# Performance work log

Measured on AMD Instinct MI355X. Metric: run time of the kernel, lower is better.

Reference implementation:

```python
import jax, jax.numpy as jnp
import numpy as np

K = 3      # spline order
NUM = 5    # grid intervals


def bspline_basis(x, grid, k=K):
    """Cox-de Boor recursion. x: (B, D); grid: (num+2k+1,) extended knots.
    Returns basis of shape (B, D, num+k)."""
    xe = x[..., None]                                       # (B, D, 1)
    B = ((xe >= grid[:-1]) & (xe < grid[1:])).astype(x.dtype)  # (B, D, num+2k)
    for p in range(1, k + 1):
        left = (xe - grid[:-(p + 1)]) / (grid[p:-1] - grid[:-(p + 1)])
        right = (grid[p + 1:] - xe) / (grid[p + 1:] - grid[1:-p])
        B = left * B[..., :-1] + right * B[..., 1:]
    return B                                                # (B, D, num+k)


def kan_layer(x, grid, coef, sb, sp, mask, bias):
    """phi(x)[b,o] = sum_i mask[o,i]*(sb[o,i]*silu(x[b,i]) + sp[o,i]*sum_c B[b,i,c]*coef[o,i,c]) + bias[o]"""
    Bsp = bspline_basis(x, grid)                            # (B, in, C)
    spline = jnp.einsum('bic,oic->bo', Bsp, coef * (sp * mask)[:, :, None])
    base = jnp.einsum('bi,oi->bo', jax.nn.silu(x), sb * mask)
    return base + spline + bias


def setup_inputs() -> dict:
    key = jax.random.key(0)
    ks = jax.random.split(key, 6)
    Bch, d0, d1, d2 = 8192, 1024, 2048, 1024
    C = NUM + K                                 # 8 spline coeffs per edge
    h = 2.0 / NUM                               # grid_range [-1,1]
    # extended knot vector: k extra knots each side, num+2k+1 = 12 points
    grid = jnp.arange(-K, NUM + K + 1, dtype=jnp.float32) * h - 1.0
    return {
        "x": jax.random.normal(ks[0], (Bch, d0), jnp.float32) * 0.5,
        "coef0": jax.random.normal(ks[1], (d1, d0, C), jnp.float32) * 0.1,
        "sb0": jax.random.normal(ks[2], (d1, d0), jnp.float32) / np.sqrt(d0).astype(np.float32),
        "sp0": jnp.ones((d1, d0), jnp.float32),
        "mask0": jnp.ones((d1, d0), jnp.float32),
        "bias0": jnp.zeros((d1,), jnp.float32),
        "coef1": jax.random.normal(ks[3], (d2, d1, C), jnp.float32) * 0.1,
        "sb1": jax.random.normal(ks[4], (d2, d1), jnp.float32) / np.sqrt(d1).astype(np.float32),
        "sp1": jnp.ones((d2, d1), jnp.float32),
        "mask1": jnp.ones((d2, d1), jnp.float32),
        "bias1": jnp.zeros((d2,), jnp.float32),
        "grid": grid,
    }


def reference(x, coef0, sb0, sp0, mask0, bias0, coef1, sb1, sp1, mask1, bias1, grid):
    h1 = kan_layer(x, grid, coef0, sb0, sp0, mask0, bias0)
    out = kan_layer(h1, grid, coef1, sb1, sp1, mask1, bias1)
    return out
```

## Files before the change

kernel.cpp:

```cpp
#include <hip/hip_runtime.h>
#include <hip/hip_bf16.h>
#include <cstdint>


typedef __attribute__((ext_vector_type(8))) short short8;
typedef __attribute__((ext_vector_type(4))) short short4v;
typedef __attribute__((ext_vector_type(4))) float f32x4;

#define GLD16(gp, lp)                                                          \
  __builtin_amdgcn_global_load_lds(                                           \
      (const __attribute__((address_space(1))) unsigned int*)(gp),             \
      (__attribute__((address_space(3))) unsigned int*)(lp), 16, 0, 0)

__device__ __forceinline__ unsigned short f2bf(float f) {
  __hip_bfloat16 h = __float2bfloat16(f);
  return *reinterpret_cast<unsigned short*>(&h);
}

__global__ void prep_w(const float* __restrict__ coef, const float* __restrict__ sb,
                       const float* __restrict__ sp, const float* __restrict__ mask,
                       __hip_bfloat16* __restrict__ W, int O, int I) {
  long idx = (long)blockIdx.x * blockDim.x + threadIdx.x;
  long total = (long)O * I;
  if (idx >= total) return;
  int i = (int)(idx % I);
  int o = (int)(idx / I);
  float mk  = mask[idx];
  float spm = sp[idx] * mk;
  float sbm = sb[idx] * mk;
  const float4* cf = (const float4*)(coef + (size_t)idx * 8);
  float4 c0 = cf[0], c1 = cf[1];
  __hip_bfloat16* base = W + (size_t)o * (size_t)(9 * I) + (i >> 5) * 288 + (i & 31);
  base[0 * 32] = __float2bfloat16(c0.x * spm);
  base[1 * 32] = __float2bfloat16(c0.y * spm);
  base[2 * 32] = __float2bfloat16(c0.z * spm);
  base[3 * 32] = __float2bfloat16(c0.w * spm);
  base[4 * 32] = __float2bfloat16(c1.x * spm);
  base[5 * 32] = __float2bfloat16(c1.y * spm);
  base[6 * 32] = __float2bfloat16(c1.z * spm);
  base[7 * 32] = __float2bfloat16(c1.w * spm);
  base[8 * 32] = __float2bfloat16(sbm);
}

__device__ __forceinline__ void basis8(float x, float* w, int& j) {
  float u  = (x + 2.2f) * 2.5f;
  float fj = floorf(u);
  j = (int)fj;
  float t  = u - fj;
  float omt = 1.0f - t;
  float t2 = t * t, t3 = t2 * t;
  w[0] = omt * omt * omt * (1.0f / 6.0f);
  w[1] = (3.0f * t3 - 6.0f * t2 + 4.0f) * (1.0f / 6.0f);
  w[2] = (-3.0f * t3 + 3.0f * t2 + 3.0f * t + 1.0f) * (1.0f / 6.0f);
  w[3] = t3 * (1.0f / 6.0f);
}

__global__ void expand_aug(const float* __restrict__ src,
                           __hip_bfloat16* __restrict__ aug,
                           long totalQuads, int I) {
  long idx = (long)blockIdx.x * blockDim.x + threadIdx.x;
  if (idx >= totalQuads) return;
  int  qtr = I >> 2;
  int  iq = (int)(idx % qtr);
  long b  = idx / qtr;
  int  i  = iq << 2;
  float4 xv = *(const float4*)(src + b * (size_t)I + i);

  float w[4][4], s[4];
  int   j[4];
#pragma unroll
  for (int e = 0; e < 4; e++) {
    float xe = (e == 0) ? xv.x : (e == 1) ? xv.y : (e == 2) ? xv.z : xv.w;
    s[e] = xe / (1.0f + __expf(-xe));
    basis8(xe, w[e], j[e]);
  }

  __hip_bfloat16* base = aug + b * (size_t)(9 * I) + (i >> 5) * 288 + (i & 31);
#pragma unroll
  for (int c = 0; c < 8; c++) {
    short4v pk;
#pragma unroll
    for (int e = 0; e < 4; e++) {
      int d = j[e] - c;
      float v = 0.0f;
      v = (d == 0) ? w[e][3] : v;
      v = (d == 1) ? w[e][2] : v;
      v = (d == 2) ? w[e][1] : v;
      v = (d == 3) ? w[e][0] : v;
      pk[e] = (short)f2bf(v);
    }
    *(short4v*)(base + c * 32) = pk;
  }
  short4v ps;
#pragma unroll
  for (int e = 0; e < 4; e++) ps[e] = (short)f2bf(s[e]);
  *(short4v*)(base + 8 * 32) = ps;
}

template <int BN>
__global__ __launch_bounds__(512, 2) void gemm8p(
    const __hip_bfloat16* __restrict__ A, const __hip_bfloat16* __restrict__ Bw,
    const float* __restrict__ bias, float* __restrict__ Cout, int N, int K) {
  constexpr int WN   = BN / 4;
  constexpr int NREP = BN / 64;
  constexpr int BNB  = BN * 64;
  constexpr int BUFB = 16384 + BNB;
  __shared__ __attribute__((aligned(16))) char lds[3 * BUFB];

  const int t = threadIdx.x;
  const int w = t >> 6, l = t & 63;
  const int wr = w >> 2, wc = w & 3;
  const int lr = l & 15;
  const int kbs = ((l >> 4) * 16) ^ (((lr >> 1) & 3) << 4);

  unsigned nwg = gridDim.x * gridDim.y;
  unsigned lin = blockIdx.y * gridDim.x + blockIdx.x;
  unsigned swz = (lin & 7) * (nwg >> 3) + (lin >> 3);
  unsigned bx = swz % gridDim.x, by = swz / gridDim.x;
  size_t brow = (size_t)by * 256, bcol = (size_t)bx * BN;

  f32x4 acc[8][NREP];
#pragma unroll
  for (int m = 0; m < 8; m++)
#pragma unroll
    for (int n = 0; n < NREP; n++) acc[m][n] = (f32x4){0.f, 0.f, 0.f, 0.f};

  const int srow  = t >> 2;
  const int scolb = ((t & 3) * 16) ^ (((srow >> 1) & 3) << 4);
  const __hip_bfloat16* gA0 = A + (brow + srow) * (size_t)K + (scolb >> 1);
  const __hip_bfloat16* gA1 = gA0 + (size_t)128 * K;
  const __hip_bfloat16* gB0 = Bw + (bcol + srow) * (size_t)K + (scolb >> 1);
  const __hip_bfloat16* gB1 = gB0 + (size_t)128 * K;

  char* ldsp = (char*)lds;
  const int paOff = (wr * 128 + lr) * 64 + kbs;
  const int pbOff = 16384 + (wc * WN + lr) * 64 + kbs;

  auto STAGE = [&](int kt, int q) {
    const int k = kt << 5;
    char* bp = ldsp + q * BUFB;
    GLD16(gA0 + k, bp + w * 1024);
    GLD16(gA1 + k, bp + 8192 + w * 1024);
    GLD16(gB0 + k, bp + 16384 + w * 1024);
    if constexpr (BN == 256) GLD16(gB1 + k, bp + 16384 + 8192 + w * 1024);
  };

  short8 bq[NREP], aq[4];
  auto COMPUTE = [&](int q) {
    const char* pa = ldsp + q * BUFB + paOff;
    const char* pb = ldsp + q * BUFB + pbOff;
#pragma unroll
    for (int n = 0; n < NREP; n++) bq[n] = *(const short8*)(pb + n * 1024);
#pragma unroll
    for (int m = 0; m < 4; m++) aq[m] = *(const short8*)(pa + m * 1024);
    __builtin_amdgcn_s_setprio(1);
#pragma unroll
    for (int m = 0; m < 4; m++)
#pragma unroll
      for (int n = 0; n < NREP; n++)
        acc[m][n] = __builtin_amdgcn_mfma_f32_16x16x32_bf16(aq[m], bq[n], acc[m][n], 0, 0, 0);
    __builtin_amdgcn_s_setprio(0);
#pragma unroll
    for (int m = 0; m < 4; m++) aq[m] = *(const short8*)(pa + (m + 4) * 1024);
    __builtin_amdgcn_s_setprio(1);
#pragma unroll
    for (int m = 0; m < 4; m++)
#pragma unroll
      for (int n = 0; n < NREP; n++)
        acc[m + 4][n] = __builtin_amdgcn_mfma_f32_16x16x32_bf16(aq[m], bq[n], acc[m + 4][n], 0, 0, 0);
    __builtin_amdgcn_s_setprio(0);
    __builtin_amdgcn_s_barrier();
  };

  const int NT = K >> 5;

  STAGE(0, 0);
  STAGE(1, 1);

  int q0 = 0;
  for (int kt = 0; kt < NT - 2; ++kt) {
    int q2 = q0 + 2; if (q2 >= 3) q2 -= 3;
    STAGE(kt + 2, q2);
    if constexpr (BN == 256) asm volatile("s_waitcnt vmcnt(8)" ::: "memory");
    else                     asm volatile("s_waitcnt vmcnt(6)" ::: "memory");
    __builtin_amdgcn_s_barrier();
    COMPUTE(q0);
    q0 = (q0 == 2) ? 0 : q0 + 1;
  }
  if constexpr (BN == 256) asm volatile("s_waitcnt vmcnt(4)" ::: "memory");
  else                     asm volatile("s_waitcnt vmcnt(3)" ::: "memory");
  __builtin_amdgcn_s_barrier();
  COMPUTE(q0);
  q0 = (q0 == 2) ? 0 : q0 + 1;
  asm volatile("s_waitcnt vmcnt(0)" ::: "memory");
  __builtin_amdgcn_s_barrier();
  COMPUTE(q0);

  const int orow = (l >> 4) << 2;
#pragma unroll
  for (int n = 0; n < NREP; n++) {
    size_t col = bcol + (size_t)wc * WN + n * 16 + lr;
    float bv = bias[col];
#pragma unroll
    for (int m = 0; m < 8; m++) {
      size_t row = brow + (size_t)wr * 128 + m * 16 + orow;
#pragma unroll
      for (int r = 0; r < 4; r++)
        Cout[(row + r) * (size_t)N + col] = acc[m][n][r] + bv;
    }
  }
}

extern "C" void kernel_launch(void* const* d_in, const int* in_sizes, int n_in,
                              void* d_out, int out_size, void* d_ws, size_t ws_size,
                              hipStream_t stream) {
  const float* x     = (const float*)d_in[0];
  const float* coef0 = (const float*)d_in[1];
  const float* sb0   = (const float*)d_in[2];
  const float* sp0   = (const float*)d_in[3];
  const float* mask0 = (const float*)d_in[4];
  const float* bias0 = (const float*)d_in[5];
  const float* coef1 = (const float*)d_in[6];
  const float* sb1   = (const float*)d_in[7];
  const float* sp1   = (const float*)d_in[8];
  const float* mask1 = (const float*)d_in[9];
  const float* bias1 = (const float*)d_in[10];
  float* out = (float*)d_out;

  const int B = 8192, D0 = 1024, D1 = 2048, D2 = 1024;
  const int K0 = 9 * D0;
  const int K1 = 9 * D1;

  char* ws = (char*)d_ws;
  float*          h1  = (float*)ws;
  __hip_bfloat16* W   = (__hip_bfloat16*)(ws + (size_t)67108864);
  __hip_bfloat16* Aug = (__hip_bfloat16*)(ws + (size_t)104857600);

  const bool fullL1 = ws_size >= (size_t)104857600 + (size_t)B * K1 * 2;

  {
    long nw = (long)D1 * D0;
    prep_w<<<(unsigned)((nw + 255) / 256), 256, 0, stream>>>(coef0, sb0, sp0, mask0, W, D1, D0);
    long np = (long)B * (D0 / 4);
    expand_aug<<<(unsigned)((np + 255) / 256), 256, 0, stream>>>(x, Aug, np, D0);
    dim3 g0(D1 / 256, B / 256);
    gemm8p<256><<<g0, 512, 0, stream>>>(Aug, W, bias0, h1, D1, K0);
  }

  {
    long nw = (long)D2 * D1;
    prep_w<<<(unsigned)((nw + 255) / 256), 256, 0, stream>>>(coef1, sb1, sp1, mask1, W, D2, D1);
    const int CH = fullL1 ? B : 4096;
    for (int ch = 0; ch < B / CH; ch++) {
      long np = (long)CH * (D1 / 4);
      expand_aug<<<(unsigned)((np + 255) / 256), 256, 0, stream>>>(
          h1 + (size_t)ch * CH * D1, Aug, np, D1);
      dim3 g1(D2 / 128, CH / 256);
      gemm8p<128><<<g1, 512, 0, stream>>>(Aug, W, bias1,
                                          out + (size_t)ch * CH * D2, D2, K1);
    }
  }
}
```

Measured before the change: 984.1 us.

## Fuse B-spline basis expansion into GEMM A-tile generation, drop Aug buffer

```diff
diff --git a/kernel.cpp b/kernel.cpp
--- a/kernel.cpp
+++ b/kernel.cpp
@@ -16,96 +16,58 @@
   __hip_bfloat16 h = __float2bfloat16(f);
   return *reinterpret_cast<unsigned short*>(&h);
 }
+__device__ __forceinline__ unsigned int pkbf(float a, float b) {
+  unsigned int r;
+  asm("v_cvt_pk_bf16_f32 %0, %1, %2" : "=v"(r) : "v"(a), "v"(b));
+  return r;
+}
 
 __global__ void prep_w(const float* __restrict__ coef, const float* __restrict__ sb,
                        const float* __restrict__ sp, const float* __restrict__ mask,
                        __hip_bfloat16* __restrict__ W, int O, int I) {
   long idx = (long)blockIdx.x * blockDim.x + threadIdx.x;
-  long total = (long)O * I;
+  long total = (long)O * (I >> 2);
   if (idx >= total) return;
-  int i = (int)(idx % I);
-  int o = (int)(idx / I);
-  float mk  = mask[idx];
-  float spm = sp[idx] * mk;
-  float sbm = sb[idx] * mk;
-  const float4* cf = (const float4*)(coef + (size_t)idx * 8);
-  float4 c0 = cf[0], c1 = cf[1];
+  int qtr = I >> 2;
+  int iq = (int)(idx % qtr);
+  int o  = (int)(idx / qtr);
+  int i  = iq << 2;
+  size_t oi = (size_t)o * I + i;
+  float4 mk4 = *(const float4*)(mask + oi);
+  float4 sp4 = *(const float4*)(sp + oi);
+  float4 sb4 = *(const float4*)(sb + oi);
+  float spm[4] = {sp4.x * mk4.x, sp4.y * mk4.y, sp4.z * mk4.z, sp4.w * mk4.w};
+  float cf[4][8];
+  const float4* cp = (const float4*)(coef + oi * 8);
+#pragma unroll
+  for (int e = 0; e < 4; e++) {
+    float4 a = cp[e * 2], b = cp[e * 2 + 1];
+    cf[e][0] = a.x; cf[e][1] = a.y; cf[e][2] = a.z; cf[e][3] = a.w;
+    cf[e][4] = b.x; cf[e][5] = b.y; cf[e][6] = b.z; cf[e][7] = b.w;
+  }
   __hip_bfloat16* base = W + (size_t)o * (size_t)(9 * I) + (i >> 5) * 288 + (i & 31);
-  base[0 * 32] = __float2bfloat16(c0.x * spm);
-  base[1 * 32] = __float2bfloat16(c0.y * spm);
-  base[2 * 32] = __float2bfloat16(c0.z * spm);
-  base[3 * 32] = __float2bfloat16(c0.w * spm);
-  base[4 * 32] = __float2bfloat16(c1.x * spm);
-  base[5 * 32] = __float2bfloat16(c1.y * spm);
-  base[6 * 32] = __float2bfloat16(c1.z * spm);
-  base[7 * 32] = __float2bfloat16(c1.w * spm);
-  base[8 * 32] = __float2bfloat16(sbm);
-}
-
-__device__ __forceinline__ void basis8(float x, float* w, int& j) {
-  float u  = (x + 2.2f) * 2.5f;
-  float fj = floorf(u);
-  j = (int)fj;
-  float t  = u - fj;
-  float omt = 1.0f - t;
-  float t2 = t * t, t3 = t2 * t;
-  w[0] = omt * omt * omt * (1.0f / 6.0f);
-  w[1] = (3.0f * t3 - 6.0f * t2 + 4.0f) * (1.0f / 6.0f);
-  w[2] = (-3.0f * t3 + 3.0f * t2 + 3.0f * t + 1.0f) * (1.0f / 6.0f);
-  w[3] = t3 * (1.0f / 6.0f);
-}
-
-__global__ void expand_aug(const float* __restrict__ src,
-                           __hip_bfloat16* __restrict__ aug,
-                           long totalQuads, int I) {
-  long idx = (long)blockIdx.x * blockDim.x + threadIdx.x;
-  if (idx >= totalQuads) return;
-  int  qtr = I >> 2;
-  int  iq = (int)(idx % qtr);
-  long b  = idx / qtr;
-  int  i  = iq << 2;
-  float4 xv = *(const float4*)(src + b * (size_t)I + i);
-
-  float w[4][4], s[4];
-  int   j[4];
-#pragma unroll
-  for (int e = 0; e < 4; e++) {
-    float xe = (e == 0) ? xv.x : (e == 1) ? xv.y : (e == 2) ? xv.z : xv.w;
-    s[e] = xe / (1.0f + __expf(-xe));
-    basis8(xe, w[e], j[e]);
-  }
-
-  __hip_bfloat16* base = aug + b * (size_t)(9 * I) + (i >> 5) * 288 + (i & 31);
 #pragma unroll
   for (int c = 0; c < 8; c++) {
     short4v pk;
 #pragma unroll
-    for (int e = 0; e < 4; e++) {
-      int d = j[e] - c;
-      float v = 0.0f;
-      v = (d == 0) ? w[e][3] : v;
-      v = (d == 1) ? w[e][2] : v;
-      v = (d == 2) ? w[e][1] : v;
-      v = (d == 3) ? w[e][0] : v;
-      pk[e] = (short)f2bf(v);
-    }
+    for (int e = 0; e < 4; e++) pk[e] = (short)f2bf(cf[e][c] * spm[e]);
     *(short4v*)(base + c * 32) = pk;
   }
   short4v ps;
-#pragma unroll
-  for (int e = 0; e < 4; e++) ps[e] = (short)f2bf(s[e]);
+  ps[0] = (short)f2bf(sb4.x * mk4.x); ps[1] = (short)f2bf(sb4.y * mk4.y);
+  ps[2] = (short)f2bf(sb4.z * mk4.z); ps[3] = (short)f2bf(sb4.w * mk4.w);
   *(short4v*)(base + 8 * 32) = ps;
 }
 
-template <int BN>
-__global__ __launch_bounds__(512, 2) void gemm8p(
-    const __hip_bfloat16* __restrict__ A, const __hip_bfloat16* __restrict__ Bw,
-    const float* __restrict__ bias, float* __restrict__ Cout, int N, int K) {
-  constexpr int WN   = BN / 4;
-  constexpr int NREP = BN / 64;
-  constexpr int BNB  = BN * 64;
-  constexpr int BUFB = 16384 + BNB;
-  __shared__ __attribute__((aligned(16))) char lds[3 * BUFB];
+struct KState { float w[8][4]; float s[8]; int j[8]; };
+
+__global__ __launch_bounds__(512, 2) void gemm_fused(
+    const float* __restrict__ X, const __hip_bfloat16* __restrict__ Bw,
+    const float* __restrict__ bias, float* __restrict__ Cout, int N, int I) {
+  constexpr int BUFB = 8192 + 16384;
+  constexpr int XOFF = 3 * BUFB;
+  __shared__ __attribute__((aligned(16))) char lds[3 * BUFB + 16384];
+  const int K = 9 * I, NB = I >> 5, NT = 9 * NB;
 
   const int t = threadIdx.x;
   const int w = t >> 6, l = t & 63;
@@ -117,93 +79,150 @@
   unsigned lin = blockIdx.y * gridDim.x + blockIdx.x;
   unsigned swz = (lin & 7) * (nwg >> 3) + (lin >> 3);
   unsigned bx = swz % gridDim.x, by = swz / gridDim.x;
-  size_t brow = (size_t)by * 256, bcol = (size_t)bx * BN;
-
-  f32x4 acc[8][NREP];
-#pragma unroll
-  for (int m = 0; m < 8; m++)
-#pragma unroll
-    for (int n = 0; n < NREP; n++) acc[m][n] = (f32x4){0.f, 0.f, 0.f, 0.f};
+  size_t brow = (size_t)by * 128, bcol = (size_t)bx * 256;
+
+  f32x4 acc[4][4];
+#pragma unroll
+  for (int m = 0; m < 4; m++)
+#pragma unroll
+    for (int n = 0; n < 4; n++) acc[m][n] = (f32x4){0.f, 0.f, 0.f, 0.f};
 
   const int srow  = t >> 2;
   const int scolb = ((t & 3) * 16) ^ (((srow >> 1) & 3) << 4);
-  const __hip_bfloat16* gA0 = A + (brow + srow) * (size_t)K + (scolb >> 1);
-  const __hip_bfloat16* gA1 = gA0 + (size_t)128 * K;
   const __hip_bfloat16* gB0 = Bw + (bcol + srow) * (size_t)K + (scolb >> 1);
   const __hip_bfloat16* gB1 = gB0 + (size_t)128 * K;
+  const float* gX0 = X + (brow + (t >> 3)) * (size_t)I + (t & 7) * 4;
+  const float* gX1 = gX0 + (size_t)64 * I;
 
   char* ldsp = (char*)lds;
-  const int paOff = (wr * 128 + lr) * 64 + kbs;
-  const int pbOff = 16384 + (wc * WN + lr) * 64 + kbs;
-
-  auto STAGE = [&](int kt, int q) {
-    const int k = kt << 5;
-    char* bp = ldsp + q * BUFB;
-    GLD16(gA0 + k, bp + w * 1024);
-    GLD16(gA1 + k, bp + 8192 + w * 1024);
-    GLD16(gB0 + k, bp + 16384 + w * 1024);
-    if constexpr (BN == 256) GLD16(gB1 + k, bp + 16384 + 8192 + w * 1024);
-  };
-
-  short8 bq[NREP], aq[4];
+  const int paOff = (wr * 64 + lr) * 64 + kbs;
+  const int pbOff = 8192 + (wc * 64 + lr) * 64 + kbs;
+  const int awOff = (t >> 2) * 64 + (((t & 3) * 16) ^ ((((t >> 2) >> 1) & 3) << 4));
+  const int xrOff = XOFF + (t >> 2) * 128 + (t & 3) * 32;
+
+  auto STAGE_B = [&](int kt, int q) {
+    char* bp = ldsp + q * BUFB + 8192;
+    GLD16(gB0 + (kt << 5), bp + w * 1024);
+    GLD16(gB1 + (kt << 5), bp + 8192 + w * 1024);
+  };
+  auto STAGE_X = [&](int ib) {
+    GLD16(gX0 + ib * 32, ldsp + XOFF + w * 1024);
+    GLD16(gX1 + ib * 32, ldsp + XOFF + 8192 + w * 1024);
+  };
+  auto EXPAND = [&](KState& st) {
+    float4 xa = *(const float4*)(ldsp + xrOff);
+    float4 xb = *(const float4*)(ldsp + xrOff + 16);
+    float xv[8] = {xa.x, xa.y, xa.z, xa.w, xb.x, xb.y, xb.z, xb.w};
+#pragma unroll
+    for (int e = 0; e < 8; e++) {
+      float x = xv[e];
+      st.s[e] = x / (1.0f + __expf(-x));
+      float u  = (x + 2.2f) * 2.5f;
+      float fj = floorf(u);
+      int   jj = (int)fj;
+      jj = jj < -1 ? -1 : (jj > 12 ? 12 : jj);
+      st.j[e] = jj;
+      float tt = u - fj, omt = 1.0f - tt;
+      float t2 = tt * tt, t3 = t2 * tt;
+      st.w[e][0] = omt * omt * omt * (1.0f / 6.0f);
+      st.w[e][1] = (3.0f * t3 - 6.0f * t2 + 4.0f) * (1.0f / 6.0f);
+      st.w[e][2] = (-3.0f * t3 + 3.0f * t2 + 3.0f * tt + 1.0f) * (1.0f / 6.0f);
+      st.w[e][3] = t3 * (1.0f / 6.0f);
+    }
+  };
+  auto WRITEA = [&](KState& st, int cw, int q) {
+    float v[8];
+    if (cw == 8) {
+#pragma unroll
+      for (int e = 0; e < 8; e++) v[e] = st.s[e];
+    } else {
+#pragma unroll
+      for (int e = 0; e < 8; e++) {
+        int d = st.j[e] - cw;
+        float r = 0.f;
+        r = (d == 3) ? st.w[e][0] : r;
+        r = (d == 2) ? st.w[e][1] : r;
+        r = (d == 1) ? st.w[e][2] : r;
+        r = (d == 0) ? st.w[e][3] : r;
+        v[e] = r;
+      }
+    }
+    uint4 pk;
+    pk.x = pkbf(v[0], v[1]); pk.y = pkbf(v[2], v[3]);
+    pk.z = pkbf(v[4], v[5]); pk.w = pkbf(v[6], v[7]);
+    *(uint4*)(ldsp + q * BUFB + awOff) = pk;
+  };
+
+  short8 aq[4], bq[4];
   auto COMPUTE = [&](int q) {
     const char* pa = ldsp + q * BUFB + paOff;
     const char* pb = ldsp + q * BUFB + pbOff;
 #pragma unroll
-    for (int n = 0; n < NREP; n++) bq[n] = *(const short8*)(pb + n * 1024);
+    for (int n = 0; n < 4; n++) bq[n] = *(const short8*)(pb + n * 1024);
 #pragma unroll
     for (int m = 0; m < 4; m++) aq[m] = *(const short8*)(pa + m * 1024);
     __builtin_amdgcn_s_setprio(1);
 #pragma unroll
     for (int m = 0; m < 4; m++)
 #pragma unroll
-      for (int n = 0; n < NREP; n++)
+      for (int n = 0; n < 4; n++)
         acc[m][n] = __builtin_amdgcn_mfma_f32_16x16x32_bf16(aq[m], bq[n], acc[m][n], 0, 0, 0);
     __builtin_amdgcn_s_setprio(0);
-#pragma unroll
-    for (int m = 0; m < 4; m++) aq[m] = *(const short8*)(pa + (m + 4) * 1024);
-    __builtin_amdgcn_s_setprio(1);
-#pragma unroll
-    for (int m = 0; m < 4; m++)
-#pragma unroll
-      for (int n = 0; n < NREP; n++)
-        acc[m + 4][n] = __builtin_amdgcn_mfma_f32_16x16x32_bf16(aq[m], bq[n], acc[m + 4][n], 0, 0, 0);
-    __builtin_amdgcn_s_setprio(0);
-    __builtin_amdgcn_s_barrier();
-  };
-
-  const int NT = K >> 5;
-
-  STAGE(0, 0);
-  STAGE(1, 1);
-
-  int q0 = 0;
+  };
+
+  KState s0, s1;
+
+  STAGE_X(0);
+  STAGE_B(0, 0);
+  STAGE_B(1, 1);
+  asm volatile("s_waitcnt vmcnt(4)" ::: "memory");
+  __builtin_amdgcn_s_barrier();
+  EXPAND(s0);
+  WRITEA(s0, 0, 0);
+
+  int q0 = 0, c = 0, ib = 0;
   for (int kt = 0; kt < NT - 2; ++kt) {
-    int q2 = q0 + 2; if (q2 >= 3) q2 -= 3;
-    STAGE(kt + 2, q2);
-    if constexpr (BN == 256) asm volatile("s_waitcnt vmcnt(8)" ::: "memory");
-    else                     asm volatile("s_waitcnt vmcnt(6)" ::: "memory");
+    int q1 = q0 + 1; if (q1 == 3) q1 = 0;
+    int q2 = q1 + 1; if (q2 == 3) q2 = 0;
+    if (c == 4 && ib + 1 < NB) STAGE_X(ib + 1);
+    STAGE_B(kt + 2, q2);
+    int cw, pw;
+    if (c == 8) { cw = 0; pw = (ib + 1) & 1; }
+    else        { cw = c + 1; pw = ib & 1; }
+    if (pw == 0) WRITEA(s0, cw, q1); else WRITEA(s1, cw, q1);
+    if (c == 7 && ib + 1 < NB) {
+      if (((ib + 1) & 1) == 0) EXPAND(s0); else EXPAND(s1);
+    }
+    asm volatile("s_waitcnt vmcnt(4) lgkmcnt(0)" ::: "memory");
     __builtin_amdgcn_s_barrier();
     COMPUTE(q0);
-    q0 = (q0 == 2) ? 0 : q0 + 1;
-  }
-  if constexpr (BN == 256) asm volatile("s_waitcnt vmcnt(4)" ::: "memory");
-  else                     asm volatile("s_waitcnt vmcnt(3)" ::: "memory");
-  __builtin_amdgcn_s_barrier();
-  COMPUTE(q0);
-  q0 = (q0 == 2) ? 0 : q0 + 1;
-  asm volatile("s_waitcnt vmcnt(0)" ::: "memory");
-  __builtin_amdgcn_s_barrier();
-  COMPUTE(q0);
+    __builtin_amdgcn_s_barrier();
+    q0 = q1;
+    if (++c == 9) { c = 0; ++ib; }
+  }
+  {
+    int q1 = q0 + 1; if (q1 == 3) q1 = 0;
+    if ((ib & 1) == 0) WRITEA(s0, 8, q1); else WRITEA(s1, 8, q1);
+    asm volatile("s_waitcnt vmcnt(2) lgkmcnt(0)" ::: "memory");
+    __builtin_amdgcn_s_barrier();
+    COMPUTE(q0);
+    __builtin_amdgcn_s_barrier();
+    q0 = q1;
+  }
+  {
+    asm volatile("s_waitcnt vmcnt(0) lgkmcnt(0)" ::: "memory");
+    __builtin_amdgcn_s_barrier();
+    COMPUTE(q0);
+  }
 
   const int orow = (l >> 4) << 2;
 #pragma unroll
-  for (int n = 0; n < NREP; n++) {
-    size_t col = bcol + (size_t)wc * WN + n * 16 + lr;
+  for (int n = 0; n < 4; n++) {
+    size_t col = bcol + (size_t)wc * 64 + n * 16 + lr;
     float bv = bias[col];
 #pragma unroll
-    for (int m = 0; m < 8; m++) {
-      size_t row = brow + (size_t)wr * 128 + m * 16 + orow;
+    for (int m = 0; m < 4; m++) {
+      size_t row = brow + (size_t)wr * 64 + m * 16 + orow;
 #pragma unroll
       for (int r = 0; r < 4; r++)
         Cout[(row + r) * (size_t)N + col] = acc[m][n][r] + bv;
@@ -228,36 +247,21 @@
   float* out = (float*)d_out;
 
   const int B = 8192, D0 = 1024, D1 = 2048, D2 = 1024;
-  const int K0 = 9 * D0;
-  const int K1 = 9 * D1;
 
   char* ws = (char*)d_ws;
-  float*          h1  = (float*)ws;
-  __hip_bfloat16* W   = (__hip_bfloat16*)(ws + (size_t)67108864);
-  __hip_bfloat16* Aug = (__hip_bfloat16*)(ws + (size_t)104857600);
-
-  const bool fullL1 = ws_size >= (size_t)104857600 + (size_t)B * K1 * 2;
-
-  {
-    long nw = (long)D1 * D0;
-    prep_w<<<(unsigned)((nw + 255) / 256), 256, 0, stream>>>(coef0, sb0, sp0, mask0, W, D1, D0);
-    long np = (long)B * (D0 / 4);
-    expand_aug<<<(unsigned)((np + 255) / 256), 256, 0, stream>>>(x, Aug, np, D0);
-    dim3 g0(D1 / 256, B / 256);
-    gemm8p<256><<<g0, 512, 0, stream>>>(Aug, W, bias0, h1, D1, K0);
-  }
-
-  {
-    long nw = (long)D2 * D1;
-    prep_w<<<(unsigned)((nw + 255) / 256), 256, 0, stream>>>(coef1, sb1, sp1, mask1, W, D2, D1);
-    const int CH = fullL1 ? B : 4096;
-    for (int ch = 0; ch < B / CH; ch++) {
-      long np = (long)CH * (D1 / 4);
-      expand_aug<<<(unsigned)((np + 255) / 256), 256, 0, stream>>>(
-          h1 + (size_t)ch * CH * D1, Aug, np, D1);
-      dim3 g1(D2 / 128, CH / 256);
-      gemm8p<128><<<g1, 512, 0, stream>>>(Aug, W, bias1,
-                                          out + (size_t)ch * CH * D2, D2, K1);
-    }
-  }
-}
+  float*          h1 = (float*)ws;
+  __hip_bfloat16* W  = (__hip_bfloat16*)(ws + (size_t)67108864);
+
+  {
+    long nt = (long)D1 * (D0 / 4);
+    prep_w<<<(unsigned)((nt + 255) / 256), 256, 0, stream>>>(coef0, sb0, sp0, mask0, W, D1, D0);
+    dim3 g0(D1 / 256, B / 128);
+    gemm_fused<<<g0, 512, 0, stream>>>(x, W, bias0, h1, D1, D0);
+  }
+  {
+    long nt = (long)D2 * (D1 / 4);
+    prep_w<<<(unsigned)((nt + 255) / 256), 256, 0, stream>>>(coef1, sb1, sp1, mask1, W, D2, D1);
+    dim3 g1(D2 / 256, B / 128);
+    gemm_fused<<<g1, 512, 0, stream>>>(h1, W, bias1, out, D2, D1);
+  }
+}
```

Measured after the change: 1.377 ms. +39.9%, slower.

## Use K=64 GEMM tiles with double buffering and widen prep/expand kernels

Applied to the files above, without the earlier changes.

```diff
diff --git a/kernel.cpp b/kernel.cpp
--- a/kernel.cpp
+++ b/kernel.cpp
@@ -21,25 +21,37 @@
                        const float* __restrict__ sp, const float* __restrict__ mask,
                        __hip_bfloat16* __restrict__ W, int O, int I) {
   long idx = (long)blockIdx.x * blockDim.x + threadIdx.x;
-  long total = (long)O * I;
+  long total = (long)O * (I >> 2);
   if (idx >= total) return;
-  int i = (int)(idx % I);
-  int o = (int)(idx / I);
-  float mk  = mask[idx];
-  float spm = sp[idx] * mk;
-  float sbm = sb[idx] * mk;
-  const float4* cf = (const float4*)(coef + (size_t)idx * 8);
-  float4 c0 = cf[0], c1 = cf[1];
+  int qtr = I >> 2;
+  int iq = (int)(idx % qtr);
+  int o  = (int)(idx / qtr);
+  int i  = iq << 2;
+  size_t oi = (size_t)o * I + i;
+  float4 mk4 = *(const float4*)(mask + oi);
+  float4 sp4 = *(const float4*)(sp + oi);
+  float4 sb4 = *(const float4*)(sb + oi);
+  float spm[4] = {sp4.x * mk4.x, sp4.y * mk4.y, sp4.z * mk4.z, sp4.w * mk4.w};
+  float cf[4][8];
+  const float4* cp = (const float4*)(coef + oi * 8);
+#pragma unroll
+  for (int e = 0; e < 4; e++) {
+    float4 a = cp[e * 2], b = cp[e * 2 + 1];
+    cf[e][0] = a.x; cf[e][1] = a.y; cf[e][2] = a.z; cf[e][3] = a.w;
+    cf[e][4] = b.x; cf[e][5] = b.y; cf[e][6] = b.z; cf[e][7] = b.w;
+  }
   __hip_bfloat16* base = W + (size_t)o * (size_t)(9 * I) + (i >> 5) * 288 + (i & 31);
-  base[0 * 32] = __float2bfloat16(c0.x * spm);
-  base[1 * 32] = __float2bfloat16(c0.y * spm);
-  base[2 * 32] = __float2bfloat16(c0.z * spm);
-  base[3 * 32] = __float2bfloat16(c0.w * spm);
-  base[4 * 32] = __float2bfloat16(c1.x * spm);
-  base[5 * 32] = __float2bfloat16(c1.y * spm);
-  base[6 * 32] = __float2bfloat16(c1.z * spm);
-  base[7 * 32] = __float2bfloat16(c1.w * spm);
-  base[8 * 32] = __float2bfloat16(sbm);
+#pragma unroll
+  for (int c = 0; c < 8; c++) {
+    short4v pk;
+#pragma unroll
+    for (int e = 0; e < 4; e++) pk[e] = (short)f2bf(cf[e][c] * spm[e]);
+    *(short4v*)(base + c * 32) = pk;
+  }
+  short4v ps;
+  ps[0] = (short)f2bf(sb4.x * mk4.x); ps[1] = (short)f2bf(sb4.y * mk4.y);
+  ps[2] = (short)f2bf(sb4.z * mk4.z); ps[3] = (short)f2bf(sb4.w * mk4.w);
+  *(short4v*)(base + 8 * 32) = ps;
 }
 
 __device__ __forceinline__ void basis8(float x, float* w, int& j) {
@@ -57,20 +69,23 @@
 
 __global__ void expand_aug(const float* __restrict__ src,
                            __hip_bfloat16* __restrict__ aug,
-                           long totalQuads, int I) {
+                           long totalOcts, int I) {
   long idx = (long)blockIdx.x * blockDim.x + threadIdx.x;
-  if (idx >= totalQuads) return;
-  int  qtr = I >> 2;
-  int  iq = (int)(idx % qtr);
-  long b  = idx / qtr;
-  int  i  = iq << 2;
-  float4 xv = *(const float4*)(src + b * (size_t)I + i);
-
-  float w[4][4], s[4];
-  int   j[4];
-#pragma unroll
-  for (int e = 0; e < 4; e++) {
-    float xe = (e == 0) ? xv.x : (e == 1) ? xv.y : (e == 2) ? xv.z : xv.w;
+  if (idx >= totalOcts) return;
+  int  oct = I >> 3;
+  int  io = (int)(idx % oct);
+  long b  = idx / oct;
+  int  i  = io << 3;
+  const float* sp = src + b * (size_t)I + i;
+  float4 xa = *(const float4*)sp;
+  float4 xb = *(const float4*)(sp + 4);
+  float xv[8] = {xa.x, xa.y, xa.z, xa.w, xb.x, xb.y, xb.z, xb.w};
+
+  float w[8][4], s[8];
+  int   j[8];
+#pragma unroll
+  for (int e = 0; e < 8; e++) {
+    float xe = xv[e];
     s[e] = xe / (1.0f + __expf(-xe));
     basis8(xe, w[e], j[e]);
   }
@@ -78,9 +93,9 @@
   __hip_bfloat16* base = aug + b * (size_t)(9 * I) + (i >> 5) * 288 + (i & 31);
 #pragma unroll
   for (int c = 0; c < 8; c++) {
-    short4v pk;
-#pragma unroll
-    for (int e = 0; e < 4; e++) {
+    short8 pk;
+#pragma unroll
+    for (int e = 0; e < 8; e++) {
       int d = j[e] - c;
       float v = 0.0f;
       v = (d == 0) ? w[e][3] : v;
@@ -89,29 +104,30 @@
       v = (d == 3) ? w[e][0] : v;
       pk[e] = (short)f2bf(v);
     }
-    *(short4v*)(base + c * 32) = pk;
-  }
-  short4v ps;
-#pragma unroll
-  for (int e = 0; e < 4; e++) ps[e] = (short)f2bf(s[e]);
-  *(short4v*)(base + 8 * 32) = ps;
+    *(short8*)(base + c * 32) = pk;
+  }
+  short8 ps;
+#pragma unroll
+  for (int e = 0; e < 8; e++) ps[e] = (short)f2bf(s[e]);
+  *(short8*)(base + 8 * 32) = ps;
 }
 
 template <int BN>
-__global__ __launch_bounds__(512, 2) void gemm8p(
+__global__ __launch_bounds__(512, 2) void gemm64(
     const __hip_bfloat16* __restrict__ A, const __hip_bfloat16* __restrict__ Bw,
     const float* __restrict__ bias, float* __restrict__ Cout, int N, int K) {
   constexpr int WN   = BN / 4;
   constexpr int NREP = BN / 64;
-  constexpr int BNB  = BN * 64;
-  constexpr int BUFB = 16384 + BNB;
-  __shared__ __attribute__((aligned(16))) char lds[3 * BUFB];
+  constexpr int BGLD = BN / 64;
+  constexpr int BUFB = 32768 + BN * 128;
+  constexpr int L    = 4 + BGLD;
+  __shared__ __attribute__((aligned(16))) char lds[2 * BUFB];
 
   const int t = threadIdx.x;
   const int w = t >> 6, l = t & 63;
   const int wr = w >> 2, wc = w & 3;
   const int lr = l & 15;
-  const int kbs = ((l >> 4) * 16) ^ (((lr >> 1) & 3) << 4);
+  const int slot0 = ((l >> 4) ^ (lr & 7)) << 4;
 
   unsigned nwg = gridDim.x * gridDim.y;
   unsigned lin = blockIdx.y * gridDim.x + blockIdx.x;
@@ -125,76 +141,78 @@
 #pragma unroll
     for (int n = 0; n < NREP; n++) acc[m][n] = (f32x4){0.f, 0.f, 0.f, 0.f};
 
-  const int srow  = t >> 2;
-  const int scolb = ((t & 3) * 16) ^ (((srow >> 1) & 3) << 4);
-  const __hip_bfloat16* gA0 = A + (brow + srow) * (size_t)K + (scolb >> 1);
-  const __hip_bfloat16* gA1 = gA0 + (size_t)128 * K;
-  const __hip_bfloat16* gB0 = Bw + (bcol + srow) * (size_t)K + (scolb >> 1);
-  const __hip_bfloat16* gB1 = gB0 + (size_t)128 * K;
+  const int ssl = (((t & 7) ^ ((t >> 3) & 7)) << 3);
+  const __hip_bfloat16* gA = A + (brow + (t >> 3)) * (size_t)K + ssl;
+  const __hip_bfloat16* gB = Bw + (bcol + (t >> 3)) * (size_t)K + ssl;
+  const size_t rs64 = (size_t)64 * K;
 
   char* ldsp = (char*)lds;
-  const int paOff = (wr * 128 + lr) * 64 + kbs;
-  const int pbOff = 16384 + (wc * WN + lr) * 64 + kbs;
 
   auto STAGE = [&](int kt, int q) {
-    const int k = kt << 5;
+    const int k = kt << 6;
     char* bp = ldsp + q * BUFB;
-    GLD16(gA0 + k, bp + w * 1024);
-    GLD16(gA1 + k, bp + 8192 + w * 1024);
-    GLD16(gB0 + k, bp + 16384 + w * 1024);
-    if constexpr (BN == 256) GLD16(gB1 + k, bp + 16384 + 8192 + w * 1024);
+#pragma unroll
+    for (int g = 0; g < 4; g++) GLD16(gA + g * rs64 + k, bp + g * 8192 + t * 16);
+#pragma unroll
+    for (int g = 0; g < BGLD; g++)
+      GLD16(gB + g * rs64 + k, bp + 32768 + g * 8192 + t * 16);
   };
 
-  short8 bq[NREP], aq[4];
   auto COMPUTE = [&](int q) {
-    const char* pa = ldsp + q * BUFB + paOff;
-    const char* pb = ldsp + q * BUFB + pbOff;
-#pragma unroll
-    for (int n = 0; n < NREP; n++) bq[n] = *(const short8*)(pb + n * 1024);
-#pragma unroll
-    for (int m = 0; m < 4; m++) aq[m] = *(const short8*)(pa + m * 1024);
-    __builtin_amdgcn_s_setprio(1);
-#pragma unroll
-    for (int m = 0; m < 4; m++)
+    const char* bb = ldsp + q * BUFB;
+    const int pa0 = (wr * 128 + lr) * 128 + slot0;
+    const int pb0 = 32768 + (wc * WN + lr) * 128 + slot0;
+#pragma unroll
+    for (int kh = 0; kh < 2; kh++) {
+      const int kx = kh ? 64 : 0;
+      short8 bq[NREP], aq[4];
 #pragma unroll
       for (int n = 0; n < NREP; n++)
-        acc[m][n] = __builtin_amdgcn_mfma_f32_16x16x32_bf16(aq[m], bq[n], acc[m][n], 0, 0, 0);
-    __builtin_amdgcn_s_setprio(0);
-#pragma unroll
-    for (int m = 0; m < 4; m++) aq[m] = *(const short8*)(pa + (m + 4) * 1024);
-    __builtin_amdgcn_s_setprio(1);
-#pragma unroll
-    for (int m = 0; m < 4; m++)
-#pragma unroll
-      for (int n = 0; n < NREP; n++)
-        acc[m + 4][n] = __builtin_amdgcn_mfma_f32_16x16x32_bf16(aq[m], bq[n], acc[m + 4][n], 0, 0, 0);
-    __builtin_amdgcn_s_setprio(0);
-    __builtin_amdgcn_s_barrier();
+        bq[n] = *(const short8*)(bb + ((pb0 + n * 2048) ^ kx));
+#pragma unroll
+      for (int m = 0; m < 4; m++)
+        aq[m] = *(const short8*)(bb + ((pa0 + m * 2048) ^ kx));
+      __builtin_amdgcn_s_setprio(1);
+#pragma unroll
+      for (int m = 0; m < 4; m++)
+#pragma unroll
+        for (int n = 0; n < NREP; n++)
+          acc[m][n] = __builtin_amdgcn_mfma_f32_16x16x32_bf16(aq[m], bq[n], acc[m][n], 0, 0, 0);
+      __builtin_amdgcn_s_setprio(0);
+#pragma unroll
+      for (int m = 0; m < 4; m++)
+        aq[m] = *(const short8*)(bb + ((pa0 + (m + 4) * 2048) ^ kx));
+      __builtin_amdgcn_s_setprio(1);
+#pragma unroll
+      for (int m = 0; m < 4; m++)
+#pragma unroll
+        for (int n = 0; n < NREP; n++)
+          acc[m + 4][n] = __builtin_amdgcn_mfma_f32_16x16x32_bf16(aq[m], bq[n], acc[m + 4][n], 0, 0, 0);
+      __builtin_amdgcn_s_setprio(0);
+    }
   };
 
-  const int NT = K >> 5;
+  const int NT = K >> 6;
 
   STAGE(0, 0);
   STAGE(1, 1);
-
-  int q0 = 0;
-  for (int kt = 0; kt < NT - 2; ++kt) {
-    int q2 = q0 + 2; if (q2 >= 3) q2 -= 3;
-    STAGE(kt + 2, q2);
-    if constexpr (BN == 256) asm volatile("s_waitcnt vmcnt(8)" ::: "memory");
-    else                     asm volatile("s_waitcnt vmcnt(6)" ::: "memory");
+  if constexpr (BN == 256) asm volatile("s_waitcnt vmcnt(8)" ::: "memory");
+  else                     asm volatile("s_waitcnt vmcnt(6)" ::: "memory");
+  __builtin_amdgcn_s_barrier();
+
+  for (int tt = 0; tt < NT; ++tt) {
+    COMPUTE(tt & 1);
     __builtin_amdgcn_s_barrier();
-    COMPUTE(q0);
-    q0 = (q0 == 2) ? 0 : q0 + 1;
-  }
-  if constexpr (BN == 256) asm volatile("s_waitcnt vmcnt(4)" ::: "memory");
-  else                     asm volatile("s_waitcnt vmcnt(3)" ::: "memory");
-  __builtin_amdgcn_s_barrier();
-  COMPUTE(q0);
-  q0 = (q0 == 2) ? 0 : q0 + 1;
-  asm volatile("s_waitcnt vmcnt(0)" ::: "memory");
-  __builtin_amdgcn_s_barrier();
-  COMPUTE(q0);
+    if (tt + 2 < NT) {
+      STAGE(tt + 2, tt & 1);
+      if constexpr (BN == 256) asm volatile("s_waitcnt vmcnt(8)" ::: "memory");
+      else                     asm volatile("s_waitcnt vmcnt(6)" ::: "memory");
+      __builtin_amdgcn_s_barrier();
+    } else if (tt + 1 < NT) {
+      asm volatile("s_waitcnt vmcnt(0)" ::: "memory");
+      __builtin_amdgcn_s_barrier();
+    }
+  }
 
   const int orow = (l >> 4) << 2;
 #pragma unroll
@@ -239,24 +257,24 @@
   const bool fullL1 = ws_size >= (size_t)104857600 + (size_t)B * K1 * 2;
 
   {
-    long nw = (long)D1 * D0;
-    prep_w<<<(unsigned)((nw + 255) / 256), 256, 0, stream>>>(coef0, sb0, sp0, mask0, W, D1, D0);
-    long np = (long)B * (D0 / 4);
-    expand_aug<<<(unsigned)((np + 255) / 256), 256, 0, stream>>>(x, Aug, np, D0);
+    long nt = (long)D1 * (D0 / 4);
+    prep_w<<<(unsigned)((nt + 255) / 256), 256, 0, stream>>>(coef0, sb0, sp0, mask0, W, D1, D0);
+    long no = (long)B * (D0 / 8);
+    expand_aug<<<(unsigned)((no + 255) / 256), 256, 0, stream>>>(x, Aug, no, D0);
     dim3 g0(D1 / 256, B / 256);
-    gemm8p<256><<<g0, 512, 0, stream>>>(Aug, W, bias0, h1, D1, K0);
+    gemm64<256><<<g0, 512, 0, stream>>>(Aug, W, bias0, h1, D1, K0);
   }
 
   {
-    long nw = (long)D2 * D1;
-    prep_w<<<(unsigned)((nw + 255) / 256), 256, 0, stream>>>(coef1, sb1, sp1, mask1, W, D2, D1);
+    long nt = (long)D2 * (D1 / 4);
+    prep_w<<<(unsigned)((nt + 255) / 256), 256, 0, stream>>>(coef1, sb1, sp1, mask1, W, D2, D1);
     const int CH = fullL1 ? B : 4096;
     for (int ch = 0; ch < B / CH; ch++) {
-      long np = (long)CH * (D1 / 4);
-      expand_aug<<<(unsigned)((np + 255) / 256), 256, 0, stream>>>(
-          h1 + (size_t)ch * CH * D1, Aug, np, D1);
+      long no = (long)CH * (D1 / 8);
+      expand_aug<<<(unsigned)((no + 255) / 256), 256, 0, stream>>>(
+          h1 + (size_t)ch * CH * D1, Aug, no, D1);
       dim3 g1(D2 / 128, CH / 256);
-      gemm8p<128><<<g1, 512, 0, stream>>>(Aug, W, bias1,
+      gemm64<128><<<g1, 512, 0, stream>>>(Aug, W, bias1,
                                           out + (size_t)ch * CH * D2, D2, K1);
     }
   }
```

New measurement: 993.7 us. Within noise of the previous version (+1.0%).
